# Optimization experiments

Hardware: AMD Instinct MI355X
Metric: run time of the kernel (lower is better)

The kernel has to match this reference:

```python
import jax, jax.numpy as jnp
import numpy as np

N_NODES = 100000
N_EDGES = 1600000
IN_CH, HID, EMB = 128, 64, 32


def _glorot(key, shape):
    lim = np.sqrt(6.0 / (shape[0] + shape[1])).astype(np.float32)
    return jax.random.uniform(key, shape, jnp.float32, -lim, lim)


def setup_inputs() -> dict:
    key = jax.random.key(0)
    ks = jax.random.split(key, 5)
    x = jax.random.normal(ks[0], (N_NODES, IN_CH), dtype=jnp.float32)
    edges = jax.random.randint(ks[1], (2, N_EDGES), 0, N_NODES)
    W1 = _glorot(ks[2], (IN_CH, HID)); b1 = jnp.zeros((HID,), jnp.float32)
    W2 = _glorot(ks[3], (HID, EMB)); b2 = jnp.zeros((EMB,), jnp.float32)
    W3 = _glorot(ks[4], (HID, EMB)); b3 = jnp.zeros((EMB,), jnp.float32)
    return {"x": x, "edges": edges, "W1": W1, "b1": b1,
            "W2": W2, "b2": b2, "W3": W3, "b3": b3}


def reference(x, edges, W1, b1, W2, b2, W3, b3):
    N = x.shape[0]
    # GCNConv default: add self-loops, symmetric D^-1/2 A D^-1/2 normalization
    loop = jnp.arange(N, dtype=edges.dtype)
    src = jnp.concatenate([edges[0], loop])  # [E+N] message sources
    dst = jnp.concatenate([edges[1], loop])  # [E+N] message targets
    deg = jax.ops.segment_sum(jnp.ones_like(dst, dtype=x.dtype), dst, num_segments=N)
    dinv = jnp.where(deg > 0, jax.lax.rsqrt(deg), 0.0)
    norm = dinv[src] * dinv[dst]  # [E+N], cached across the three convs (cached=True)

    def gcn(h, W, b):
        h = h @ W                                  # [N, out]
        msg = h[src] * norm[:, None]               # gather + edge scale
        return jax.ops.segment_sum(msg, dst, num_segments=N) + b  # scatter-add

    h = jax.nn.relu(gcn(x, W1, b1))
    return gcn(h, W2, b2), gcn(h, W3, b3)
```

## Files before the change

kernel.cpp:

```cpp
#include <hip/hip_runtime.h>

#define NN 100000
#define NE 1600000
#define NB 391
#define CHUNK 4096
#define NCHUNK 391

typedef __attribute__((ext_vector_type(8))) short short8_t;
typedef __attribute__((ext_vector_type(4))) float float4_t;

__device__ inline unsigned short f2bf(float f) {
    unsigned int u = __float_as_uint(f);
    unsigned int r = u + 0x7fffu + ((u >> 16) & 1u);
    return (unsigned short)(r >> 16);
}
__device__ inline float bf_lo(unsigned int u) { return __uint_as_float(u << 16); }
__device__ inline float bf_hi(unsigned int u) { return __uint_as_float(u & 0xffff0000u); }

__global__ __launch_bounds__(256) void k_pre(const float* __restrict__ W1,
                                             const float* __restrict__ W2,
                                             const float* __restrict__ W3,
                                             unsigned short* __restrict__ wtb,
                                             unsigned short* __restrict__ wt2) {
    int f = blockIdx.x * 256 + threadIdx.x;
    int c = f >> 7, k = f & 127;
    wtb[f] = f2bf(W1[k * 64 + c]);
    if (f < 4096) {
        int c2 = f >> 6, k2 = f & 63;
        float v = (c2 < 32) ? W2[k2 * 32 + c2] : W3[k2 * 32 + (c2 - 32)];
        wt2[f] = f2bf(v);
    }
}

__global__ __launch_bounds__(256) void k_chist(const int* __restrict__ dst,
                                               int* __restrict__ hist2d) {
    __shared__ int lh[NB];
    int c = blockIdx.x, t = threadIdx.x;
    for (int i = t; i < NB; i += 256) lh[i] = 0;
    __syncthreads();
    int e0 = c * CHUNK, e1 = min(e0 + CHUNK, NE);
    for (int e = e0 + t; e < e1; e += 256)
        atomicAdd(&lh[dst[e] >> 8], 1);
    __syncthreads();
    for (int i = t; i < NB; i += 256) hist2d[c * NB + i] = lh[i];
}

__global__ __launch_bounds__(256) void k_scancol(const int* __restrict__ hist2d,
                                                 int* __restrict__ base2d,
                                                 int* __restrict__ colsum) {
    __shared__ int sh[256];
    int b = blockIdx.x, t = threadIdx.x;
    int base = t * 2;
    int v0 = (base + 0 < NCHUNK) ? hist2d[(base + 0) * NB + b] : 0;
    int v1 = (base + 1 < NCHUNK) ? hist2d[(base + 1) * NB + b] : 0;
    int tsum = v0 + v1;
    sh[t] = tsum;
    __syncthreads();
    for (int d = 1; d < 256; d <<= 1) {
        int x = (t >= d) ? sh[t - d] : 0;
        __syncthreads();
        sh[t] += x;
        __syncthreads();
    }
    int excl = sh[t] - tsum;
    if (base + 0 < NCHUNK) base2d[(base + 0) * NB + b] = excl;
    if (base + 1 < NCHUNK) base2d[(base + 1) * NB + b] = excl + v0;
    if (t == 255) colsum[b] = sh[255];
}

__global__ __launch_bounds__(256) void k_scanb(const int* __restrict__ colsum,
                                               int* __restrict__ boff) {
    __shared__ int sh[256];
    int t = threadIdx.x;
    int base = t * 2;
    int v0 = (base + 0 < NB) ? colsum[base + 0] : 0;
    int v1 = (base + 1 < NB) ? colsum[base + 1] : 0;
    int tsum = v0 + v1;
    sh[t] = tsum;
    __syncthreads();
    for (int d = 1; d < 256; d <<= 1) {
        int x = (t >= d) ? sh[t - d] : 0;
        __syncthreads();
        sh[t] += x;
        __syncthreads();
    }
    int excl = sh[t] - tsum;
    if (base + 0 < NB) boff[base + 0] = excl;
    if (base + 1 < NB) boff[base + 1] = excl + v0;
    if (t == 255) boff[NB] = sh[255];
}

__global__ __launch_bounds__(512, 8) void k_fuse(const float* __restrict__ x,
                                                 const unsigned short* __restrict__ wtb,
                                                 unsigned short* __restrict__ t1b,
                                                 const int* __restrict__ src,
                                                 const int* __restrict__ dst,
                                                 const int* __restrict__ base2d,
                                                 const int* __restrict__ boff,
                                                 unsigned int* __restrict__ pairs) {
    __shared__ int sbuf[2 * NB];
    const int b = blockIdx.x;
    const int t = threadIdx.x;

    if ((b % 3) == 2) {
        int* lbase = sbuf;
        int* lh    = sbuf + NB;
        const int c = b / 3;
        int e0 = c * CHUNK;
        int e1 = min(e0 + CHUNK, NE);
        for (int i = t; i < NB; i += 512) {
            lbase[i] = base2d[c * NB + i] + boff[i];
            lh[i] = 0;
        }
        __syncthreads();
        for (int e = e0 + t; e < e1; e += 512) {
            int d = dst[e];
            int bk = d >> 8;
            int r = atomicAdd(&lh[bk], 1);
            pairs[lbase[bk] + r] = (unsigned int)src[e] | ((unsigned int)(d & 255) << 17);
        }
    } else {
        const int tile = 2 * (b / 3) + (b % 3);
        const int row0 = tile * 128;
        const int nrows = min(128, NN - row0);
        const int w = t >> 6, l = t & 63;
        const int m15 = l & 15, kg = l >> 4;

        int ra = min(row0 + w * 16 + m15, NN - 1);
        const float4* xa = (const float4*)(x + (size_t)ra * 128) + kg * 2;

        float4 f[8];
        #pragma unroll
        for (int ks = 0; ks < 4; ++ks) {
            f[2 * ks]     = xa[ks * 8];
            f[2 * ks + 1] = xa[ks * 8 + 1];
        }

        float4_t acc[4];
        #pragma unroll
        for (int cb = 0; cb < 4; ++cb) acc[cb] = (float4_t){0.f, 0.f, 0.f, 0.f};

        #pragma unroll
        for (int ks = 0; ks < 4; ++ks) {
            float4 f0 = f[2 * ks], f1 = f[2 * ks + 1];
            short8_t a;
            a[0] = (short)f2bf(f0.x); a[1] = (short)f2bf(f0.y);
            a[2] = (short)f2bf(f0.z); a[3] = (short)f2bf(f0.w);
            a[4] = (short)f2bf(f1.x); a[5] = (short)f2bf(f1.y);
            a[6] = (short)f2bf(f1.z); a[7] = (short)f2bf(f1.w);
            #pragma unroll
            for (int cb = 0; cb < 4; ++cb) {
                short8_t bb = *(const short8_t*)(wtb + (cb * 16 + m15) * 128 + ks * 32 + kg * 8);
                acc[cb] = __builtin_amdgcn_mfma_f32_16x16x32_bf16(a, bb, acc[cb], 0, 0, 0);
            }
        }

        #pragma unroll
        for (int r = 0; r < 4; ++r) {
            int lrow = w * 16 + kg * 4 + r;
            if (lrow < nrows) {
                size_t grow = (size_t)(row0 + lrow);
                #pragma unroll
                for (int cb = 0; cb < 4; ++cb)
                    t1b[grow * 64 + cb * 16 + m15] = f2bf(acc[cb][r]);
            }
        }
    }
}

__global__ __launch_bounds__(256) void k_fine(const unsigned int* __restrict__ pairs,
                                              const int* __restrict__ boff,
                                              int* __restrict__ csr_off,
                                              int* __restrict__ csr_src,
                                              float* __restrict__ dinv) {
    __shared__ int lcnt[256];
    __shared__ int sc[256];
    __shared__ int lofs[256];
    int t = threadIdx.x;
    int b = blockIdx.x;
    int n0 = b << 8;
    int nnode = min(256, NN - n0);
    int bO = boff[b], bE = boff[b + 1];

    lcnt[t] = 0;
    __syncthreads();
    for (int e = bO + t; e < bE; e += 256)
        atomicAdd(&lcnt[pairs[e] >> 17], 1);
    __syncthreads();
    sc[t] = lcnt[t];
    __syncthreads();
    for (int d = 1; d < 256; d <<= 1) {
        int x = (t >= d) ? sc[t - d] : 0;
        __syncthreads();
        sc[t] += x;
        __syncthreads();
    }
    {
        int excl = sc[t] - lcnt[t];
        lofs[t] = excl;
        if (t < nnode) {
            int n = n0 + t;
            csr_off[n] = bO + excl;
            dinv[n] = rsqrtf(1.0f + (float)lcnt[t]);
        }
        lcnt[t] = 0;
    }
    if (b == NB - 1 && t == 0) csr_off[NN] = NE;
    __syncthreads();
    for (int e = bO + t; e < bE; e += 256) {
        unsigned int w = pairs[e];
        int li = (int)(w >> 17);
        int r = atomicAdd(&lcnt[li], 1);
        csr_src[bO + lofs[li] + r] = (int)(w & 0x1FFFFu);
    }
}

__global__ __launch_bounds__(256) void k_gather8(const int* __restrict__ off,
                                                 const int* __restrict__ csr,
                                                 const float* __restrict__ dinv,
                                                 const unsigned short* __restrict__ hb,
                                                 const float* __restrict__ bias,
                                                 unsigned int* __restrict__ outp) {
    int idx = blockIdx.x * 256 + threadIdx.x;
    int n = idx >> 3;
    if (n >= NN) return;
    int c8 = idx & 7;
    const uint4* h4 = (const uint4*)hb;
    float dn = dinv[n];
    float a0[8], a1[8];
    {
        uint4 v = h4[(size_t)n * 8 + c8];
        a0[0] = dn * bf_lo(v.x); a0[1] = dn * bf_hi(v.x);
        a0[2] = dn * bf_lo(v.y); a0[3] = dn * bf_hi(v.y);
        a0[4] = dn * bf_lo(v.z); a0[5] = dn * bf_hi(v.z);
        a0[6] = dn * bf_lo(v.w); a0[7] = dn * bf_hi(v.w);
        #pragma unroll
        for (int j = 0; j < 8; ++j) a1[j] = 0.f;
    }
    int b = off[n], e = off[n + 1];
    int i = b;
    for (; i + 1 < e; i += 2) {
        int s0 = csr[i], s1 = csr[i + 1];
        float w0 = dinv[s0], w1 = dinv[s1];
        uint4 v0 = h4[(size_t)s0 * 8 + c8];
        uint4 v1 = h4[(size_t)s1 * 8 + c8];
        a0[0] += w0 * bf_lo(v0.x); a0[1] += w0 * bf_hi(v0.x);
        a0[2] += w0 * bf_lo(v0.y); a0[3] += w0 * bf_hi(v0.y);
        a0[4] += w0 * bf_lo(v0.z); a0[5] += w0 * bf_hi(v0.z);
        a0[6] += w0 * bf_lo(v0.w); a0[7] += w0 * bf_hi(v0.w);
        a1[0] += w1 * bf_lo(v1.x); a1[1] += w1 * bf_hi(v1.x);
        a1[2] += w1 * bf_lo(v1.y); a1[3] += w1 * bf_hi(v1.y);
        a1[4] += w1 * bf_lo(v1.z); a1[5] += w1 * bf_hi(v1.z);
        a1[6] += w1 * bf_lo(v1.w); a1[7] += w1 * bf_hi(v1.w);
    }
    if (i < e) {
        int s = csr[i];
        float w = dinv[s];
        uint4 v = h4[(size_t)s * 8 + c8];
        a0[0] += w * bf_lo(v.x); a0[1] += w * bf_hi(v.x);
        a0[2] += w * bf_lo(v.y); a0[3] += w * bf_hi(v.y);
        a0[4] += w * bf_lo(v.z); a0[5] += w * bf_hi(v.z);
        a0[6] += w * bf_lo(v.w); a0[7] += w * bf_hi(v.w);
    }
    float4 b0 = ((const float4*)bias)[c8 * 2];
    float4 b1v = ((const float4*)bias)[c8 * 2 + 1];
    float o[8];
    o[0] = dn * fmaxf(dn * (a0[0] + a1[0]) + b0.x, 0.f);
    o[1] = dn * fmaxf(dn * (a0[1] + a1[1]) + b0.y, 0.f);
    o[2] = dn * fmaxf(dn * (a0[2] + a1[2]) + b0.z, 0.f);
    o[3] = dn * fmaxf(dn * (a0[3] + a1[3]) + b0.w, 0.f);
    o[4] = dn * fmaxf(dn * (a0[4] + a1[4]) + b1v.x, 0.f);
    o[5] = dn * fmaxf(dn * (a0[5] + a1[5]) + b1v.y, 0.f);
    o[6] = dn * fmaxf(dn * (a0[6] + a1[6]) + b1v.z, 0.f);
    o[7] = dn * fmaxf(dn * (a0[7] + a1[7]) + b1v.w, 0.f);
    uint4 p;
    p.x = (unsigned int)f2bf(o[0]) | ((unsigned int)f2bf(o[1]) << 16);
    p.y = (unsigned int)f2bf(o[2]) | ((unsigned int)f2bf(o[3]) << 16);
    p.z = (unsigned int)f2bf(o[4]) | ((unsigned int)f2bf(o[5]) << 16);
    p.w = (unsigned int)f2bf(o[6]) | ((unsigned int)f2bf(o[7]) << 16);
    ((uint4*)outp)[(size_t)n * 8 + c8] = p;
}

__global__ __launch_bounds__(512) void k_gemm23(const unsigned short* __restrict__ h1b,
                                                const unsigned short* __restrict__ wt2,
                                                unsigned short* __restrict__ y) {
    __shared__ __align__(16) unsigned short lx[128 * 72];
    __shared__ __align__(16) unsigned short lw[64 * 72];
    const int t = threadIdx.x;
    const int row0 = blockIdx.x * 128;
    const int nrows = min(128, NN - row0);

    #pragma unroll
    for (int i = 0; i < 2; ++i) {
        int f = t + i * 512;
        int r = f >> 3, c8 = f & 7;
        uint4 v = make_uint4(0u, 0u, 0u, 0u);
        if (r < nrows) v = ((const uint4*)h1b)[(size_t)(row0 + r) * 8 + c8];
        *(uint4*)&lx[r * 72 + c8 * 8] = v;
    }
    if (t < 512) {
        int c = t >> 3, c8 = t & 7;
        uint4 v = ((const uint4*)wt2)[t];
        *(uint4*)&lw[c * 72 + c8 * 8] = v;
    }
    __syncthreads();

    const int w = t >> 6, l = t & 63;
    const int m15 = l & 15, kg = l >> 4;
    const unsigned short* pa = &lx[(w * 16 + m15) * 72 + kg * 8];
    const unsigned short* pb = &lw[m15 * 72 + kg * 8];

    float4_t acc[4];
    #pragma unroll
    for (int cb = 0; cb < 4; ++cb) acc[cb] = (float4_t){0.f, 0.f, 0.f, 0.f};

    #pragma unroll
    for (int ks = 0; ks < 2; ++ks) {
        short8_t a = *(const short8_t*)(pa + ks * 32);
        #pragma unroll
        for (int cb = 0; cb < 4; ++cb) {
            short8_t bb = *(const short8_t*)(pb + cb * (16 * 72) + ks * 32);
            acc[cb] = __builtin_amdgcn_mfma_f32_16x16x32_bf16(a, bb, acc[cb], 0, 0, 0);
        }
    }

    #pragma unroll
    for (int r = 0; r < 4; ++r) {
        int lrow = w * 16 + kg * 4 + r;
        if (lrow < nrows) {
            size_t grow = (size_t)(row0 + lrow);
            #pragma unroll
            for (int cb = 0; cb < 4; ++cb)
                y[grow * 64 + cb * 16 + m15] = f2bf(acc[cb][r]);
        }
    }
}

__global__ __launch_bounds__(256) void k_gatherO(const int* __restrict__ off,
                                                 const int* __restrict__ csr,
                                                 const float* __restrict__ dinv,
                                                 const unsigned short* __restrict__ yb,
                                                 const float* __restrict__ b2,
                                                 const float* __restrict__ b3,
                                                 float* __restrict__ out) {
    int idx = blockIdx.x * 256 + threadIdx.x;
    int n = idx >> 3;
    int c8 = idx & 7;
    const uint4* h4 = (const uint4*)yb;
    float a0[8], a1[8];
    {
        uint4 v = h4[(size_t)n * 8 + c8];
        a0[0] = bf_lo(v.x); a0[1] = bf_hi(v.x);
        a0[2] = bf_lo(v.y); a0[3] = bf_hi(v.y);
        a0[4] = bf_lo(v.z); a0[5] = bf_hi(v.z);
        a0[6] = bf_lo(v.w); a0[7] = bf_hi(v.w);
        #pragma unroll
        for (int j = 0; j < 8; ++j) a1[j] = 0.f;
    }
    int b = off[n], e = off[n + 1];
    int i = b;
    for (; i + 1 < e; i += 2) {
        int s0 = csr[i], s1 = csr[i + 1];
        uint4 v0 = h4[(size_t)s0 * 8 + c8];
        uint4 v1 = h4[(size_t)s1 * 8 + c8];
        a0[0] += bf_lo(v0.x); a0[1] += bf_hi(v0.x);
        a0[2] += bf_lo(v0.y); a0[3] += bf_hi(v0.y);
        a0[4] += bf_lo(v0.z); a0[5] += bf_hi(v0.z);
        a0[6] += bf_lo(v0.w); a0[7] += bf_hi(v0.w);
        a1[0] += bf_lo(v1.x); a1[1] += bf_hi(v1.x);
        a1[2] += bf_lo(v1.y); a1[3] += bf_hi(v1.y);
        a1[4] += bf_lo(v1.z); a1[5] += bf_hi(v1.z);
        a1[6] += bf_lo(v1.w); a1[7] += bf_hi(v1.w);
    }
    if (i < e) {
        uint4 v = h4[(size_t)csr[i] * 8 + c8];
        a0[0] += bf_lo(v.x); a0[1] += bf_hi(v.x);
        a0[2] += bf_lo(v.y); a0[3] += bf_hi(v.y);
        a0[4] += bf_lo(v.z); a0[5] += bf_hi(v.z);
        a0[6] += bf_lo(v.w); a0[7] += bf_hi(v.w);
    }
    float dn = dinv[n];
    const float* bp = (c8 < 4) ? (b2 + c8 * 8) : (b3 + (c8 - 4) * 8);
    float4 q0 = *(const float4*)bp;
    float4 q1 = *(const float4*)(bp + 4);
    float4 o0, o1;
    o0.x = dn * (a0[0] + a1[0]) + q0.x;
    o0.y = dn * (a0[1] + a1[1]) + q0.y;
    o0.z = dn * (a0[2] + a1[2]) + q0.z;
    o0.w = dn * (a0[3] + a1[3]) + q0.w;
    o1.x = dn * (a0[4] + a1[4]) + q1.x;
    o1.y = dn * (a0[5] + a1[5]) + q1.y;
    o1.z = dn * (a0[6] + a1[6]) + q1.z;
    o1.w = dn * (a0[7] + a1[7]) + q1.w;
    float* op = (c8 < 4) ? (out + (size_t)n * 32 + c8 * 8)
                         : (out + (size_t)NN * 32 + (size_t)n * 32 + (c8 - 4) * 8);
    *(float4*)op = o0;
    *(float4*)(op + 4) = o1;
}

extern "C" void kernel_launch(void* const* d_in, const int* in_sizes, int n_in,
                              void* d_out, int out_size, void* d_ws, size_t ws_size,
                              hipStream_t stream) {
    const float* x  = (const float*)d_in[0];
    const int* edges = (const int*)d_in[1];
    const float* W1 = (const float*)d_in[2];
    const float* b1 = (const float*)d_in[3];
    const float* W2 = (const float*)d_in[4];
    const float* b2 = (const float*)d_in[5];
    const float* W3 = (const float*)d_in[6];
    const float* b3 = (const float*)d_in[7];
    float* out = (float*)d_out;

    const int* srcs = edges;
    const int* dsts = edges + NE;

    int*   csr_off = (int*)d_ws;
    float* dinv    = (float*)((int*)d_ws + 100004);
    int*   csr_src = (int*)d_ws + 200004;
    int*   colsum  = (int*)d_ws + 1800004;
    int*   boff    = (int*)d_ws + 1800396;
    unsigned short* wtb = (unsigned short*)((int*)d_ws + 1800800);
    unsigned short* t1b = (unsigned short*)((int*)d_ws + 1804896);
    unsigned short* y   = t1b;
    unsigned int*   pairs  = (unsigned int*)((int*)d_ws + 5004896);
    int*            hist2d = (int*)d_ws + 5004896 + 1600000;
    int*            base2d = (int*)d_ws + 5004896 + 1752896;
    unsigned short* h1b    = (unsigned short*)pairs;
    unsigned short* wt2 = (unsigned short*)(out + 6400000 - 2048);

    dim3 blk(256);
    const int gN8 = (NN * 8 + 255) / 256;
    const int gT23 = (NN + 127) / 128;

    k_pre<<<32, blk, 0, stream>>>(W1, W2, W3, wtb, wt2);
    k_chist<<<NCHUNK, blk, 0, stream>>>(dsts, hist2d);
    k_scancol<<<NB, blk, 0, stream>>>(hist2d, base2d, colsum);
    k_scanb<<<1, blk, 0, stream>>>(colsum, boff);

    k_fuse<<<3 * NCHUNK, dim3(512), 0, stream>>>(x, wtb, t1b, srcs, dsts,
                                                 base2d, boff, pairs);

    k_fine<<<NB, blk, 0, stream>>>(pairs, boff, csr_off, csr_src, dinv);

    k_gather8<<<gN8, blk, 0, stream>>>(csr_off, csr_src, dinv, t1b, b1,
                                       (unsigned int*)h1b);
    k_gemm23<<<gT23, dim3(512), 0, stream>>>(h1b, wt2, y);
    k_gatherO<<<gN8, blk, 0, stream>>>(csr_off, csr_src, dinv, y, b2, b3, out);
}
```

Baseline: 148.5 us.

## Fuse second-layer GEMM into first aggregation kernel via shuffles and LDS weights

The MFMA-based k_gemm23 kernel is removed. The first-layer gather now multiplies each node's 64-wide hidden row by the combined W2|W3 matrix held in LDS, sharing hidden values across the 8 lanes of a node with shuffles. This drops the round trip of the bf16 hidden activations through global memory and one launch. In exchange the GEMM runs on scalar FMA instead of MFMA, adding 64x8 FMAs per thread in a kernel that was memory-bound. The weight layout in k_pre is transposed to match, and the early return for n >= NN is removed because __shfl needs every lane present.

```diff
diff --git a/kernel.cpp b/kernel.cpp
--- a/kernel.cpp
+++ b/kernel.cpp
@@ -26,7 +26,7 @@
     int c = f >> 7, k = f & 127;
     wtb[f] = f2bf(W1[k * 64 + c]);
     if (f < 4096) {
-        int c2 = f >> 6, k2 = f & 63;
+        int k2 = f >> 6, c2 = f & 63;
         float v = (c2 < 32) ? W2[k2 * 32 + c2] : W3[k2 * 32 + (c2 - 32)];
         wt2[f] = f2bf(v);
     }
@@ -215,15 +215,24 @@
     }
 }
 
-__global__ __launch_bounds__(256) void k_gather8(const int* __restrict__ off,
-                                                 const int* __restrict__ csr,
-                                                 const float* __restrict__ dinv,
-                                                 const unsigned short* __restrict__ hb,
-                                                 const float* __restrict__ bias,
-                                                 unsigned int* __restrict__ outp) {
+__global__ __launch_bounds__(256, 8) void k_gatherY(const int* __restrict__ off,
+                                                    const int* __restrict__ csr,
+                                                    const float* __restrict__ dinv,
+                                                    const unsigned short* __restrict__ hb,
+                                                    const float* __restrict__ bias,
+                                                    const unsigned short* __restrict__ wt2,
+                                                    unsigned int* __restrict__ yp) {
+    __shared__ __align__(16) unsigned short lw[64 * 64];
+    #pragma unroll
+    for (int i = 0; i < 2; ++i) {
+        int f = threadIdx.x + i * 256;
+        uint4 v = ((const uint4*)wt2)[f];
+        *(uint4*)&lw[f * 8] = v;
+    }
+    __syncthreads();
+
     int idx = blockIdx.x * 256 + threadIdx.x;
     int n = idx >> 3;
-    if (n >= NN) return;
     int c8 = idx & 7;
     const uint4* h4 = (const uint4*)hb;
     float dn = dinv[n];
@@ -273,67 +282,33 @@
     o[5] = dn * fmaxf(dn * (a0[5] + a1[5]) + b1v.y, 0.f);
     o[6] = dn * fmaxf(dn * (a0[6] + a1[6]) + b1v.z, 0.f);
     o[7] = dn * fmaxf(dn * (a0[7] + a1[7]) + b1v.w, 0.f);
+
+    const int lbase = threadIdx.x & 56;
+    float yv[8];
+    #pragma unroll
+    for (int j = 0; j < 8; ++j) yv[j] = 0.f;
+    #pragma unroll
+    for (int g = 0; g < 8; ++g) {
+        float hq[8];
+        #pragma unroll
+        for (int j = 0; j < 8; ++j) hq[j] = __shfl(o[j], lbase + g);
+        #pragma unroll
+        for (int j = 0; j < 8; ++j) {
+            int k = g * 8 + j;
+            uint4 wv = *(const uint4*)&lw[k * 64 + c8 * 8];
+            float h = hq[j];
+            yv[0] += h * bf_lo(wv.x); yv[1] += h * bf_hi(wv.x);
+            yv[2] += h * bf_lo(wv.y); yv[3] += h * bf_hi(wv.y);
+            yv[4] += h * bf_lo(wv.z); yv[5] += h * bf_hi(wv.z);
+            yv[6] += h * bf_lo(wv.w); yv[7] += h * bf_hi(wv.w);
+        }
+    }
     uint4 p;
-    p.x = (unsigned int)f2bf(o[0]) | ((unsigned int)f2bf(o[1]) << 16);
-    p.y = (unsigned int)f2bf(o[2]) | ((unsigned int)f2bf(o[3]) << 16);
-    p.z = (unsigned int)f2bf(o[4]) | ((unsigned int)f2bf(o[5]) << 16);
-    p.w = (unsigned int)f2bf(o[6]) | ((unsigned int)f2bf(o[7]) << 16);
-    ((uint4*)outp)[(size_t)n * 8 + c8] = p;
-}
-
-__global__ __launch_bounds__(512) void k_gemm23(const unsigned short* __restrict__ h1b,
-                                                const unsigned short* __restrict__ wt2,
-                                                unsigned short* __restrict__ y) {
-    __shared__ __align__(16) unsigned short lx[128 * 72];
-    __shared__ __align__(16) unsigned short lw[64 * 72];
-    const int t = threadIdx.x;
-    const int row0 = blockIdx.x * 128;
-    const int nrows = min(128, NN - row0);
-
-    #pragma unroll
-    for (int i = 0; i < 2; ++i) {
-        int f = t + i * 512;
-        int r = f >> 3, c8 = f & 7;
-        uint4 v = make_uint4(0u, 0u, 0u, 0u);
-        if (r < nrows) v = ((const uint4*)h1b)[(size_t)(row0 + r) * 8 + c8];
-        *(uint4*)&lx[r * 72 + c8 * 8] = v;
-    }
-    if (t < 512) {
-        int c = t >> 3, c8 = t & 7;
-        uint4 v = ((const uint4*)wt2)[t];
-        *(uint4*)&lw[c * 72 + c8 * 8] = v;
-    }
-    __syncthreads();
-
-    const int w = t >> 6, l = t & 63;
-    const int m15 = l & 15, kg = l >> 4;
-    const unsigned short* pa = &lx[(w * 16 + m15) * 72 + kg * 8];
-    const unsigned short* pb = &lw[m15 * 72 + kg * 8];
-
-    float4_t acc[4];
-    #pragma unroll
-    for (int cb = 0; cb < 4; ++cb) acc[cb] = (float4_t){0.f, 0.f, 0.f, 0.f};
-
-    #pragma unroll
-    for (int ks = 0; ks < 2; ++ks) {
-        short8_t a = *(const short8_t*)(pa + ks * 32);
-        #pragma unroll
-        for (int cb = 0; cb < 4; ++cb) {
-            short8_t bb = *(const short8_t*)(pb + cb * (16 * 72) + ks * 32);
-            acc[cb] = __builtin_amdgcn_mfma_f32_16x16x32_bf16(a, bb, acc[cb], 0, 0, 0);
-        }
-    }
-
-    #pragma unroll
-    for (int r = 0; r < 4; ++r) {
-        int lrow = w * 16 + kg * 4 + r;
-        if (lrow < nrows) {
-            size_t grow = (size_t)(row0 + lrow);
-            #pragma unroll
-            for (int cb = 0; cb < 4; ++cb)
-                y[grow * 64 + cb * 16 + m15] = f2bf(acc[cb][r]);
-        }
-    }
+    p.x = (unsigned int)f2bf(yv[0]) | ((unsigned int)f2bf(yv[1]) << 16);
+    p.y = (unsigned int)f2bf(yv[2]) | ((unsigned int)f2bf(yv[3]) << 16);
+    p.z = (unsigned int)f2bf(yv[4]) | ((unsigned int)f2bf(yv[5]) << 16);
+    p.w = (unsigned int)f2bf(yv[6]) | ((unsigned int)f2bf(yv[7]) << 16);
+    ((uint4*)yp)[(size_t)n * 8 + c8] = p;
 }
 
 __global__ __launch_bounds__(256) void k_gatherO(const int* __restrict__ off,
@@ -421,16 +396,14 @@
     int*   boff    = (int*)d_ws + 1800396;
     unsigned short* wtb = (unsigned short*)((int*)d_ws + 1800800);
     unsigned short* t1b = (unsigned short*)((int*)d_ws + 1804896);
-    unsigned short* y   = t1b;
     unsigned int*   pairs  = (unsigned int*)((int*)d_ws + 5004896);
     int*            hist2d = (int*)d_ws + 5004896 + 1600000;
     int*            base2d = (int*)d_ws + 5004896 + 1752896;
-    unsigned short* h1b    = (unsigned short*)pairs;
+    unsigned short* y      = (unsigned short*)pairs;
     unsigned short* wt2 = (unsigned short*)(out + 6400000 - 2048);
 
     dim3 blk(256);
     const int gN8 = (NN * 8 + 255) / 256;
-    const int gT23 = (NN + 127) / 128;
 
     k_pre<<<32, blk, 0, stream>>>(W1, W2, W3, wtb, wt2);
     k_chist<<<NCHUNK, blk, 0, stream>>>(dsts, hist2d);
@@ -442,8 +415,7 @@
 
     k_fine<<<NB, blk, 0, stream>>>(pairs, boff, csr_off, csr_src, dinv);
 
-    k_gather8<<<gN8, blk, 0, stream>>>(csr_off, csr_src, dinv, t1b, b1,
-                                       (unsigned int*)h1b);
-    k_gemm23<<<gT23, dim3(512), 0, stream>>>(h1b, wt2, y);
+    k_gatherY<<<gN8, blk, 0, stream>>>(csr_off, csr_src, dinv, t1b, b1, wt2,
+                                       (unsigned int*)y);
     k_gatherO<<<gN8, blk, 0, stream>>>(csr_off, csr_src, dinv, y, b2, b3, out);
 }
```

Result: no change. 149.8 us (+0.9%).
